# Kernel optimization log

Hardware: AMD Instinct MI355X
Metric: run time of the kernel (lower is better)

Reference implementation:

```python
import jax, jax.numpy as jnp
import numpy as np

MASK_THRESH = 0.9
USED_PENALTY = 1e8


def setup_inputs() -> dict:
    key = jax.random.key(0)
    k1, k2, k3, k4 = jax.random.split(key, 4)
    B, C, H, W = 16, 1, 128, 128
    P, L = 16, 6            # num_protos, num_objects
    T = P * L               # candidate templates per image
    x = jax.random.uniform(k1, (B, C, H, W), jnp.float32)
    templates = jax.random.uniform(k2, (B, T, C, H, W), jnp.float32)
    masks = jax.random.uniform(k3, (B, T, 1, H, W), jnp.float32)
    background = jax.random.uniform(k4, (C, H, W), jnp.float32)
    return {"x": x, "templates": templates, "masks": masks,
            "background": background, "num_objects": L}


def reference(x, templates, masks, background, num_objects):
    """Greedy template selection (use_empty=True) + scene composition.

    Faithful to DecompModel4._greedy_selection + compose_templates:
    at each of L steps, every candidate template is composed UNDER the
    already-selected objects (compose paints last index first), the MSE vs
    the image is computed, the argmin candidate is selected, and non-empty
    candidates are masked out for future steps. Final reconstruction paints
    selected objects over the background with object 0 on top.
    """
    B, T, C, H, W = templates.shape
    L = num_objects
    dt = templates.dtype

    # prepend the empty template (index 0), as in use_empty=True
    temps = jnp.concatenate([jnp.zeros((B, 1, C, H, W), dt), templates], axis=1)  # (B,T+1,C,H,W)
    msks = jnp.concatenate([jnp.zeros((B, 1, 1, H, W), dt), masks], axis=1)       # (B,T+1,1,H,W)
    Tp1 = T + 1
    bidx = jnp.arange(B)
    bg = background[None]                      # (1,C,H,W)

    # candidate-over-background image, constant across greedy steps
    cand_cov = msks > MASK_THRESH              # (B,T+1,1,H,W)
    cand_img = jnp.where(cand_cov, temps * msks, bg[:, None])  # (B,T+1,C,H,W)

    # running canvas of already-selected objects (earlier selections on top)
    used = jnp.zeros((B, Tp1), bool)
    top_val = jnp.zeros((B, C, H, W), dt)
    top_cov = jnp.zeros((B, 1, H, W), bool)

    for _ in range(L):
        # selected stack painted over each candidate-over-background
        cur = jnp.where(top_cov[:, None], top_val[:, None], cand_img)  # (B,T+1,C,H,W)
        err = jnp.mean((x[:, None] - cur) ** 2, axis=(2, 3, 4))        # (B,T+1)
        err = jnp.where(used, USED_PENALTY, err)
        cid = jnp.argmin(err, axis=1)                                  # (B,)
        # mark as used, except the empty template (id 0) stays reusable
        used = used | ((jnp.arange(Tp1)[None, :] == cid[:, None]) & (cid != 0)[:, None])
        sel_obj = temps[bidx, cid]     # (B,C,H,W)
        sel_msk = msks[bidx, cid]      # (B,1,H,W)
        new_cov = sel_msk > MASK_THRESH
        # new selection goes UNDER already-selected pixels
        top_val = jnp.where((~top_cov) & new_cov, sel_obj * sel_msk, top_val)
        top_cov = top_cov | new_cov

    reconstruction = jnp.where(top_cov, top_val, bg)   # (B,C,H,W)
    return reconstruction
```

## Files before the change

### kernel.cpp

```cpp
#include <hip/hip_runtime.h>

#define B    16
#define T    96
#define TP1  97
#define HW   16384
#define HW4  4096
#define LSEL 6
#define THRESH 0.9f
#define SEG  512
#define CAP  2048

#define WS_CONTRIB 0
#define WS_USED    8192
#define WS_COUNTS  16384
#define WS_COV     41984
#define WS_CIDX    304128
#define WS_CVAL    6595584
#define WS_NEEDED  (WS_CVAL + (size_t)B * T * CAP * 4)

__global__ __launch_bounds__(256) void compact_kernel(
    const float* __restrict__ x, const float* __restrict__ temps,
    const float* __restrict__ msks, const float* __restrict__ bg,
    unsigned short* __restrict__ cidx, float* __restrict__ cval,
    int* __restrict__ counts, float* __restrict__ contrib)
{
    int slot = blockIdx.x;
    int b = slot / T, t = slot - b * T;
    const float4* t4  = ((const float4*)temps) + (size_t)slot * HW4;
    const float4* m4  = ((const float4*)msks)  + (size_t)slot * HW4;
    const float4* x4  = ((const float4*)x)     + (size_t)b * HW4;
    const float4* bg4 = (const float4*)bg;
    int wv = threadIdx.x >> 6, lane = threadIdx.x & 63;
    unsigned long long below = lane ? (~0ULL >> (64 - lane)) : 0ULL;
    unsigned short* sidx = cidx + (size_t)slot * CAP + wv * SEG;
    float*          sval = cval + (size_t)slot * CAP + wv * SEG;

    int off = 0;
    float sum = 0.f;
    int ib = wv * 1024 + lane;

    #pragma unroll
    for (int it = 0; it < 16; it += 4) {
        float4 tv[4], mv[4], xv[4], bv[4];
        #pragma unroll
        for (int u = 0; u < 4; ++u) {
            int i = ib + (it + u) * 64;
            tv[u] = t4[i]; mv[u] = m4[i]; xv[u] = x4[i]; bv[u] = bg4[i];
        }
        #pragma unroll
        for (int u = 0; u < 4; ++u) {
            int pix = (ib + (it + u) * 64) * 4;
            bool p0 = mv[u].x > THRESH, p1 = mv[u].y > THRESH,
                 p2 = mv[u].z > THRESH, p3 = mv[u].w > THRESH;
            float a0 = xv[u].x - tv[u].x * mv[u].x, c0 = xv[u].x - bv[u].x;
            float a1 = xv[u].y - tv[u].y * mv[u].y, c1 = xv[u].y - bv[u].y;
            float a2 = xv[u].z - tv[u].z * mv[u].z, c2 = xv[u].z - bv[u].z;
            float a3 = xv[u].w - tv[u].w * mv[u].w, c3 = xv[u].w - bv[u].w;
            float v0 = a0*a0 - c0*c0, v1 = a1*a1 - c1*c1;
            float v2 = a2*a2 - c2*c2, v3 = a3*a3 - c3*c3;
            unsigned long long B0 = __ballot(p0), B1 = __ballot(p1);
            unsigned long long B2 = __ballot(p2), B3 = __ballot(p3);
            int n0 = __popcll(B0), n1 = __popcll(B1), n2 = __popcll(B2), n3 = __popcll(B3);
            if (p0) { int pos = off + __popcll(B0 & below);
                      if (pos < SEG) { sidx[pos] = (unsigned short)(pix+0); sval[pos] = v0; sum += v0; } }
            if (p1) { int pos = off + n0 + __popcll(B1 & below);
                      if (pos < SEG) { sidx[pos] = (unsigned short)(pix+1); sval[pos] = v1; sum += v1; } }
            if (p2) { int pos = off + n0 + n1 + __popcll(B2 & below);
                      if (pos < SEG) { sidx[pos] = (unsigned short)(pix+2); sval[pos] = v2; sum += v2; } }
            if (p3) { int pos = off + n0 + n1 + n2 + __popcll(B3 & below);
                      if (pos < SEG) { sidx[pos] = (unsigned short)(pix+3); sval[pos] = v3; sum += v3; } }
            off += n0 + n1 + n2 + n3;
        }
    }

    #pragma unroll
    for (int o = 32; o > 0; o >>= 1) sum += __shfl_down(sum, o, 64);
    __shared__ float s[4];
    if (lane == 0) s[wv] = sum;
    __syncthreads();
    if (threadIdx.x == 0) contrib[b * TP1 + t + 1] = s[0] + s[1] + s[2] + s[3];
    if (lane == 0) counts[slot * 4 + wv] = (off < SEG) ? off : SEG;
}

__global__ __launch_bounds__(256) void step_contrib_kernel(
    const unsigned short* __restrict__ cidx, const float* __restrict__ cval,
    const int* __restrict__ counts, const unsigned char* __restrict__ top_cov,
    float* __restrict__ contrib)
{
    int slot = blockIdx.x;
    int b = slot / T, t = slot - b * T;
    int wv = threadIdx.x >> 6, lane = threadIdx.x & 63;
    int n = counts[slot * 4 + wv];
    const unsigned short* sidx = cidx + (size_t)slot * CAP + wv * SEG;
    const float*          sval = cval + (size_t)slot * CAP + wv * SEG;
    const unsigned char*  cov  = top_cov + (size_t)b * HW;

    float sum = 0.f;
    for (int i = lane; i < n; i += 64) {
        unsigned short p = sidx[i];
        float v = sval[i];
        if (!cov[p]) sum += v;
    }
    #pragma unroll
    for (int o = 32; o > 0; o >>= 1) sum += __shfl_down(sum, o, 64);
    __shared__ float s[4];
    if (lane == 0) s[wv] = sum;
    __syncthreads();
    if (threadIdx.x == 0) contrib[b * TP1 + t + 1] = s[0] + s[1] + s[2] + s[3];
}

__global__ __launch_bounds__(256) void sel_upd_kernel(
    const float* __restrict__ contrib, const float* __restrict__ temps,
    const float* __restrict__ msks, const float* __restrict__ bg,
    unsigned long long* __restrict__ used, unsigned char* __restrict__ top_cov,
    float* __restrict__ out, int first, int last)
{
    int b = blockIdx.y, g = blockIdx.x;
    int tid = threadIdx.x;
    __shared__ float sv[128];
    __shared__ int   si[128];
    __shared__ int   sc;
    if (tid < 128) {
        float v = 3.0e38f;
        if (tid < TP1) {
            if (tid == 0) v = 0.0f;
            else {
                v = contrib[b * TP1 + tid];
                if (!first && ((used[b * 2 + (tid >> 6)] >> (tid & 63)) & 1ULL)) v = 1.0e8f;
            }
        }
        sv[tid] = v; si[tid] = tid;
    }
    __syncthreads();
    for (int o = 64; o > 0; o >>= 1) {
        if (tid < o) {
            float v2 = sv[tid + o]; int i2 = si[tid + o];
            if (v2 < sv[tid] || (v2 == sv[tid] && i2 < si[tid])) { sv[tid] = v2; si[tid] = i2; }
        }
        __syncthreads();
    }
    if (tid == 0) sc = si[0];
    __syncthreads();
    int c = sc;

    if (!last && g == 0 && tid == 0) {
        if (first) {
            used[b * 2 + 0] = (c != 0 && c < 64) ? (1ULL << c) : 0ULL;
            used[b * 2 + 1] = (c >= 64) ? (1ULL << (c - 64)) : 0ULL;
        } else if (c != 0) {
            atomicOr(&used[b * 2 + (c >> 6)], 1ULL << (c & 63));
        }
    }

    uchar4* covp = (uchar4*)(top_cov + (size_t)b * HW);
    float4* valp = (float4*)(out + (size_t)b * HW);
    const float4* bg4 = (const float4*)bg;
    int k0 = g * 1024;

    if (!last) {
        if (c != 0) {
            size_t tb = (size_t)(b * T + c - 1) * HW4;
            const float4* t4 = ((const float4*)temps) + tb;
            const float4* m4 = ((const float4*)msks) + tb;
            for (int k = k0 + tid; k < k0 + 1024; k += 256) {
                float4 mv = m4[k], tv = t4[k];
                uchar4 cv; float4 vv;
                if (first) {
                    cv.x = mv.x > THRESH; cv.y = mv.y > THRESH;
                    cv.z = mv.z > THRESH; cv.w = mv.w > THRESH;
                    vv.x = tv.x * mv.x; vv.y = tv.y * mv.y;
                    vv.z = tv.z * mv.z; vv.w = tv.w * mv.w;
                } else {
                    cv = covp[k]; vv = valp[k];
                    if (mv.x > THRESH && !cv.x) { vv.x = tv.x * mv.x; cv.x = 1; }
                    if (mv.y > THRESH && !cv.y) { vv.y = tv.y * mv.y; cv.y = 1; }
                    if (mv.z > THRESH && !cv.z) { vv.z = tv.z * mv.z; cv.z = 1; }
                    if (mv.w > THRESH && !cv.w) { vv.w = tv.w * mv.w; cv.w = 1; }
                }
                covp[k] = cv; valp[k] = vv;
            }
        } else if (first) {
            for (int k = k0 + tid; k < k0 + 1024; k += 256)
                covp[k] = make_uchar4(0, 0, 0, 0);
        }
    } else {
        if (c != 0) {
            size_t tb = (size_t)(b * T + c - 1) * HW4;
            const float4* t4 = ((const float4*)temps) + tb;
            const float4* m4 = ((const float4*)msks) + tb;
            for (int k = k0 + tid; k < k0 + 1024; k += 256) {
                float4 mv = m4[k], tv = t4[k];
                uchar4 cv = covp[k];
                float4 vv = valp[k];
                float4 bv = bg4[k];
                vv.x = cv.x ? vv.x : (mv.x > THRESH ? tv.x * mv.x : bv.x);
                vv.y = cv.y ? vv.y : (mv.y > THRESH ? tv.y * mv.y : bv.y);
                vv.z = cv.z ? vv.z : (mv.z > THRESH ? tv.z * mv.z : bv.z);
                vv.w = cv.w ? vv.w : (mv.w > THRESH ? tv.w * mv.w : bv.w);
                valp[k] = vv;
            }
        } else {
            for (int k = k0 + tid; k < k0 + 1024; k += 256) {
                uchar4 cv = covp[k];
                float4 vv = valp[k];
                float4 bv = bg4[k];
                if (!cv.x) vv.x = bv.x;
                if (!cv.y) vv.y = bv.y;
                if (!cv.z) vv.z = bv.z;
                if (!cv.w) vv.w = bv.w;
                valp[k] = vv;
            }
        }
    }
}

__global__ __launch_bounds__(256) void contrib_full_kernel(
    const float* __restrict__ x, const float* __restrict__ temps,
    const float* __restrict__ msks, const float* __restrict__ bg,
    const unsigned char* __restrict__ top_cov, float* __restrict__ contrib,
    int first)
{
    int b = blockIdx.x / T;
    int t = blockIdx.x % T;
    size_t base = (size_t)(b * T + t) * HW;
    const float4* t4  = (const float4*)(temps + base);
    const float4* m4  = (const float4*)(msks + base);
    const float4* x4  = (const float4*)(x + (size_t)b * HW);
    const float4* bg4 = (const float4*)bg;
    const uchar4* c4  = (const uchar4*)(top_cov + (size_t)b * HW);
    float sum = 0.f;
    #pragma unroll 4
    for (int i = threadIdx.x; i < HW4; i += 256) {
        float4 tv = t4[i], mv = m4[i], xv = x4[i], bv = bg4[i];
        uchar4 cv = first ? make_uchar4(0,0,0,0) : c4[i];
        if (mv.x > THRESH && !cv.x) { float d1 = xv.x - tv.x*mv.x, d2 = xv.x - bv.x; sum += d1*d1 - d2*d2; }
        if (mv.y > THRESH && !cv.y) { float d1 = xv.y - tv.y*mv.y, d2 = xv.y - bv.y; sum += d1*d1 - d2*d2; }
        if (mv.z > THRESH && !cv.z) { float d1 = xv.z - tv.z*mv.z, d2 = xv.z - bv.z; sum += d1*d1 - d2*d2; }
        if (mv.w > THRESH && !cv.w) { float d1 = xv.w - tv.w*mv.w, d2 = xv.w - bv.w; sum += d1*d1 - d2*d2; }
    }
    #pragma unroll
    for (int o = 32; o > 0; o >>= 1) sum += __shfl_down(sum, o, 64);
    __shared__ float s[4];
    int lane = threadIdx.x & 63, wid = threadIdx.x >> 6;
    if (lane == 0) s[wid] = sum;
    __syncthreads();
    if (threadIdx.x == 0)
        contrib[b * TP1 + t + 1] = s[0] + s[1] + s[2] + s[3];
}

extern "C" void kernel_launch(void* const* d_in, const int* in_sizes, int n_in,
                              void* d_out, int out_size, void* d_ws, size_t ws_size,
                              hipStream_t stream) {
    const float* x     = (const float*)d_in[0];
    const float* temps = (const float*)d_in[1];
    const float* msks  = (const float*)d_in[2];
    const float* bg    = (const float*)d_in[3];

    char* ws = (char*)d_ws;
    float*              contrib = (float*)(ws + WS_CONTRIB);
    unsigned long long* used    = (unsigned long long*)(ws + WS_USED);
    int*                counts  = (int*)(ws + WS_COUNTS);
    unsigned char*      top_cov = (unsigned char*)(ws + WS_COV);
    unsigned short*     cidx    = (unsigned short*)(ws + WS_CIDX);
    float*              cval    = (float*)(ws + WS_CVAL);
    float*              out     = (float*)d_out;

    if (ws_size >= WS_NEEDED) {
        compact_kernel<<<B * T, 256, 0, stream>>>(x, temps, msks, bg,
                                                  cidx, cval, counts, contrib);
        sel_upd_kernel<<<dim3(4, B), 256, 0, stream>>>(contrib, temps, msks, bg,
                                                       used, top_cov, out, 1, 0);
        for (int l = 1; l < LSEL - 1; ++l) {
            step_contrib_kernel<<<B * T, 256, 0, stream>>>(cidx, cval, counts, top_cov, contrib);
            sel_upd_kernel<<<dim3(4, B), 256, 0, stream>>>(contrib, temps, msks, bg,
                                                           used, top_cov, out, 0, 0);
        }
        step_contrib_kernel<<<B * T, 256, 0, stream>>>(cidx, cval, counts, top_cov, contrib);
        sel_upd_kernel<<<dim3(4, B), 256, 0, stream>>>(contrib, temps, msks, bg,
                                                       used, top_cov, out, 0, 1);
    } else {
        contrib_full_kernel<<<B * T, 256, 0, stream>>>(x, temps, msks, bg, top_cov, contrib, 1);
        sel_upd_kernel<<<dim3(4, B), 256, 0, stream>>>(contrib, temps, msks, bg,
                                                       used, top_cov, out, 1, 0);
        for (int l = 1; l < LSEL - 1; ++l) {
            contrib_full_kernel<<<B * T, 256, 0, stream>>>(x, temps, msks, bg, top_cov, contrib, 0);
            sel_upd_kernel<<<dim3(4, B), 256, 0, stream>>>(contrib, temps, msks, bg,
                                                           used, top_cov, out, 0, 0);
        }
        contrib_full_kernel<<<B * T, 256, 0, stream>>>(x, temps, msks, bg, top_cov, contrib, 0);
        sel_upd_kernel<<<dim3(4, B), 256, 0, stream>>>(contrib, temps, msks, bg,
                                                       used, top_cov, out, 0, 1);
    }
}
```

Baseline: 300.1 us.

## Fuse greedy selection into one persistent kernel with grid barriers

```diff
diff --git a/kernel.cpp b/kernel.cpp
--- a/kernel.cpp
+++ b/kernel.cpp
@@ -7,210 +7,232 @@
 #define HW4  4096
 #define LSEL 6
 #define THRESH 0.9f
-#define SEG  512
-#define CAP  2048
-
-#define WS_CONTRIB 0
-#define WS_USED    8192
-#define WS_COUNTS  16384
-#define WS_COV     41984
-#define WS_CIDX    304128
-#define WS_CVAL    6595584
-#define WS_NEEDED  (WS_CVAL + (size_t)B * T * CAP * 4)
-
-__global__ __launch_bounds__(256) void compact_kernel(
+#define SCAP  2048
+#define NBLK  256
+#define NSLOT (B * T)
+
+#define WS_BAR     0
+#define WS_SCOUNT  1024
+#define WS_CONTRIB 8192
+#define WS_USEDT   14848
+#define WS_COV     24576
+#define WS_CIDX    286720
+#define WS_CVAL    6578176
+#define WS_NEEDED  19161088ULL
+
+__global__ void init_kernel(unsigned long long* bar, unsigned* scount) {
+    int i = blockIdx.x * blockDim.x + threadIdx.x;
+    if (i < NSLOT) scount[i] = 0u;
+    if (i == 0) *bar = 0ULL;
+}
+
+__device__ __forceinline__ void grid_barrier(unsigned long long* bar,
+                                             unsigned long long target) {
+    __syncthreads();
+    __threadfence();
+    if (threadIdx.x == 0) {
+        __hip_atomic_fetch_add(bar, 1ULL, __ATOMIC_RELEASE, __HIP_MEMORY_SCOPE_AGENT);
+        while (__hip_atomic_load(bar, __ATOMIC_ACQUIRE, __HIP_MEMORY_SCOPE_AGENT) < target)
+            __builtin_amdgcn_s_sleep(2);
+    }
+    __syncthreads();
+    __threadfence();
+}
+
+__global__ __launch_bounds__(256, 1) void coop_kernel(
     const float* __restrict__ x, const float* __restrict__ temps,
     const float* __restrict__ msks, const float* __restrict__ bg,
     unsigned short* __restrict__ cidx, float* __restrict__ cval,
-    int* __restrict__ counts, float* __restrict__ contrib)
+    unsigned* __restrict__ scount, float* __restrict__ contrib,
+    unsigned char* __restrict__ cov, float* __restrict__ out,
+    unsigned long long* __restrict__ bar)
 {
-    int slot = blockIdx.x;
-    int b = slot / T, t = slot - b * T;
-    const float4* t4  = ((const float4*)temps) + (size_t)slot * HW4;
-    const float4* m4  = ((const float4*)msks)  + (size_t)slot * HW4;
-    const float4* x4  = ((const float4*)x)     + (size_t)b * HW4;
-    const float4* bg4 = (const float4*)bg;
-    int wv = threadIdx.x >> 6, lane = threadIdx.x & 63;
-    unsigned long long below = lane ? (~0ULL >> (64 - lane)) : 0ULL;
-    unsigned short* sidx = cidx + (size_t)slot * CAP + wv * SEG;
-    float*          sval = cval + (size_t)slot * CAP + wv * SEG;
-
-    int off = 0;
-    float sum = 0.f;
-    int ib = wv * 1024 + lane;
-
-    #pragma unroll
-    for (int it = 0; it < 16; it += 4) {
-        float4 tv[4], mv[4], xv[4], bv[4];
-        #pragma unroll
-        for (int u = 0; u < 4; ++u) {
-            int i = ib + (it + u) * 64;
-            tv[u] = t4[i]; mv[u] = m4[i]; xv[u] = x4[i]; bv[u] = bg4[i];
-        }
-        #pragma unroll
-        for (int u = 0; u < 4; ++u) {
-            int pix = (ib + (it + u) * 64) * 4;
-            bool p0 = mv[u].x > THRESH, p1 = mv[u].y > THRESH,
-                 p2 = mv[u].z > THRESH, p3 = mv[u].w > THRESH;
-            float a0 = xv[u].x - tv[u].x * mv[u].x, c0 = xv[u].x - bv[u].x;
-            float a1 = xv[u].y - tv[u].y * mv[u].y, c1 = xv[u].y - bv[u].y;
-            float a2 = xv[u].z - tv[u].z * mv[u].z, c2 = xv[u].z - bv[u].z;
-            float a3 = xv[u].w - tv[u].w * mv[u].w, c3 = xv[u].w - bv[u].w;
-            float v0 = a0*a0 - c0*c0, v1 = a1*a1 - c1*c1;
-            float v2 = a2*a2 - c2*c2, v3 = a3*a3 - c3*c3;
-            unsigned long long B0 = __ballot(p0), B1 = __ballot(p1);
-            unsigned long long B2 = __ballot(p2), B3 = __ballot(p3);
-            int n0 = __popcll(B0), n1 = __popcll(B1), n2 = __popcll(B2), n3 = __popcll(B3);
-            if (p0) { int pos = off + __popcll(B0 & below);
-                      if (pos < SEG) { sidx[pos] = (unsigned short)(pix+0); sval[pos] = v0; sum += v0; } }
-            if (p1) { int pos = off + n0 + __popcll(B1 & below);
-                      if (pos < SEG) { sidx[pos] = (unsigned short)(pix+1); sval[pos] = v1; sum += v1; } }
-            if (p2) { int pos = off + n0 + n1 + __popcll(B2 & below);
-                      if (pos < SEG) { sidx[pos] = (unsigned short)(pix+2); sval[pos] = v2; sum += v2; } }
-            if (p3) { int pos = off + n0 + n1 + n2 + __popcll(B3 & below);
-                      if (pos < SEG) { sidx[pos] = (unsigned short)(pix+3); sval[pos] = v3; sum += v3; } }
-            off += n0 + n1 + n2 + n3;
-        }
-    }
-
-    #pragma unroll
-    for (int o = 32; o > 0; o >>= 1) sum += __shfl_down(sum, o, 64);
-    __shared__ float s[4];
-    if (lane == 0) s[wv] = sum;
-    __syncthreads();
-    if (threadIdx.x == 0) contrib[b * TP1 + t + 1] = s[0] + s[1] + s[2] + s[3];
-    if (lane == 0) counts[slot * 4 + wv] = (off < SEG) ? off : SEG;
-}
-
-__global__ __launch_bounds__(256) void step_contrib_kernel(
-    const unsigned short* __restrict__ cidx, const float* __restrict__ cval,
-    const int* __restrict__ counts, const unsigned char* __restrict__ top_cov,
-    float* __restrict__ contrib)
-{
-    int slot = blockIdx.x;
-    int b = slot / T, t = slot - b * T;
-    int wv = threadIdx.x >> 6, lane = threadIdx.x & 63;
-    int n = counts[slot * 4 + wv];
-    const unsigned short* sidx = cidx + (size_t)slot * CAP + wv * SEG;
-    const float*          sval = cval + (size_t)slot * CAP + wv * SEG;
-    const unsigned char*  cov  = top_cov + (size_t)b * HW;
-
-    float sum = 0.f;
-    for (int i = lane; i < n; i += 64) {
-        unsigned short p = sidx[i];
-        float v = sval[i];
-        if (!cov[p]) sum += v;
-    }
-    #pragma unroll
-    for (int o = 32; o > 0; o >>= 1) sum += __shfl_down(sum, o, 64);
-    __shared__ float s[4];
-    if (lane == 0) s[wv] = sum;
-    __syncthreads();
-    if (threadIdx.x == 0) contrib[b * TP1 + t + 1] = s[0] + s[1] + s[2] + s[3];
-}
-
-__global__ __launch_bounds__(256) void sel_upd_kernel(
-    const float* __restrict__ contrib, const float* __restrict__ temps,
-    const float* __restrict__ msks, const float* __restrict__ bg,
-    unsigned long long* __restrict__ used, unsigned char* __restrict__ top_cov,
-    float* __restrict__ out, int first, int last)
-{
-    int b = blockIdx.y, g = blockIdx.x;
-    int tid = threadIdx.x;
+    const int bid = blockIdx.x;
+    const int tid = threadIdx.x;
+    const int lane = tid & 63, wv = tid >> 6;
+    const int b = bid >> 4;
+    const int chunk = bid & 15;
+
     __shared__ float sv[128];
     __shared__ int   si[128];
-    __shared__ int   sc;
-    if (tid < 128) {
-        float v = 3.0e38f;
-        if (tid < TP1) {
-            if (tid == 0) v = 0.0f;
-            else {
-                v = contrib[b * TP1 + tid];
-                if (!first && ((used[b * 2 + (tid >> 6)] >> (tid & 63)) & 1ULL)) v = 1.0e8f;
-            }
-        }
-        sv[tid] = v; si[tid] = tid;
-    }
-    __syncthreads();
-    for (int o = 64; o > 0; o >>= 1) {
-        if (tid < o) {
-            float v2 = sv[tid + o]; int i2 = si[tid + o];
-            if (v2 < sv[tid] || (v2 == sv[tid] && i2 < si[tid])) { sv[tid] = v2; si[tid] = i2; }
-        }
-        __syncthreads();
-    }
-    if (tid == 0) sc = si[0];
-    __syncthreads();
-    int c = sc;
-
-    if (!last && g == 0 && tid == 0) {
-        if (first) {
-            used[b * 2 + 0] = (c != 0 && c < 64) ? (1ULL << c) : 0ULL;
-            used[b * 2 + 1] = (c >= 64) ? (1ULL << (c - 64)) : 0ULL;
-        } else if (c != 0) {
-            atomicOr(&used[b * 2 + (c >> 6)], 1ULL << (c & 63));
-        }
-    }
-
-    uchar4* covp = (uchar4*)(top_cov + (size_t)b * HW);
-    float4* valp = (float4*)(out + (size_t)b * HW);
-    const float4* bg4 = (const float4*)bg;
-    int k0 = g * 1024;
-
-    if (!last) {
-        if (c != 0) {
-            size_t tb = (size_t)(b * T + c - 1) * HW4;
-            const float4* t4 = ((const float4*)temps) + tb;
-            const float4* m4 = ((const float4*)msks) + tb;
-            for (int k = k0 + tid; k < k0 + 1024; k += 256) {
-                float4 mv = m4[k], tv = t4[k];
-                uchar4 cv; float4 vv;
-                if (first) {
-                    cv.x = mv.x > THRESH; cv.y = mv.y > THRESH;
-                    cv.z = mv.z > THRESH; cv.w = mv.w > THRESH;
-                    vv.x = tv.x * mv.x; vv.y = tv.y * mv.y;
-                    vv.z = tv.z * mv.z; vv.w = tv.w * mv.w;
+    __shared__ int   scid;
+    __shared__ float sr[4];
+
+    bool my_used = false;
+    unsigned long long tgt = NBLK;
+
+    {
+        const float4* x4  = (const float4*)x + (size_t)b * HW4 + chunk * 256;
+        const float4* bgp = (const float4*)bg + chunk * 256;
+        float4 xv = x4[tid];
+        float4 bv = bgp[tid];
+        float4 d2;
+        d2.x = (xv.x - bv.x) * (xv.x - bv.x);
+        d2.y = (xv.y - bv.y) * (xv.y - bv.y);
+        d2.z = (xv.z - bv.z) * (xv.z - bv.z);
+        d2.w = (xv.w - bv.w) * (xv.w - bv.w);
+
+        const unsigned long long below = lane ? (~0ULL >> (64 - lane)) : 0ULL;
+        const float4* tbase = (const float4*)temps + (size_t)(b * T) * HW4 + chunk * 256 + tid;
+        const float4* mbase = (const float4*)msks  + (size_t)(b * T) * HW4 + chunk * 256 + tid;
+        const int gpix = (chunk * 256 + tid) * 4;
+
+        #pragma unroll 1
+        for (int t0 = 0; t0 < T; t0 += 8) {
+            float4 mv[8], tv[8];
+            #pragma unroll
+            for (int u = 0; u < 8; ++u) {
+                mv[u] = mbase[(size_t)(t0 + u) * HW4];
+                tv[u] = tbase[(size_t)(t0 + u) * HW4];
+            }
+            unsigned long long Ba0[8], Ba1[8], Ba2[8], Ba3[8];
+            int n0[8], n1[8], n2[8];
+            unsigned basew[8];
+            #pragma unroll
+            for (int u = 0; u < 8; ++u) {
+                Ba0[u] = __ballot(mv[u].x > THRESH);
+                Ba1[u] = __ballot(mv[u].y > THRESH);
+                Ba2[u] = __ballot(mv[u].z > THRESH);
+                Ba3[u] = __ballot(mv[u].w > THRESH);
+                n0[u] = __popcll(Ba0[u]); n1[u] = __popcll(Ba1[u]); n2[u] = __popcll(Ba2[u]);
+                int cnt4 = n0[u] + n1[u] + n2[u] + __popcll(Ba3[u]);
+                if (lane == 0)
+                    basew[u] = atomicAdd(&scount[b * T + t0 + u], (unsigned)cnt4);
+            }
+            #pragma unroll
+            for (int u = 0; u < 8; ++u) {
+                unsigned bw = (unsigned)__shfl((int)basew[u], 0, 64);
+                int slot = b * T + t0 + u;
+                unsigned short* ci = cidx + (size_t)slot * SCAP;
+                float*          cw = cval + (size_t)slot * SCAP;
+                float a0 = xv.x - tv[u].x * mv[u].x; float v0 = a0 * a0 - d2.x;
+                float a1 = xv.y - tv[u].y * mv[u].y; float v1 = a1 * a1 - d2.y;
+                float a2 = xv.z - tv[u].z * mv[u].z; float v2 = a2 * a2 - d2.z;
+                float a3 = xv.w - tv[u].w * mv[u].w; float v3 = a3 * a3 - d2.w;
+                if (mv[u].x > THRESH) {
+                    unsigned pos = bw + __popcll(Ba0[u] & below);
+                    if (pos < SCAP) { ci[pos] = (unsigned short)(gpix + 0); cw[pos] = v0; }
+                }
+                if (mv[u].y > THRESH) {
+                    unsigned pos = bw + n0[u] + __popcll(Ba1[u] & below);
+                    if (pos < SCAP) { ci[pos] = (unsigned short)(gpix + 1); cw[pos] = v1; }
+                }
+                if (mv[u].z > THRESH) {
+                    unsigned pos = bw + n0[u] + n1[u] + __popcll(Ba2[u] & below);
+                    if (pos < SCAP) { ci[pos] = (unsigned short)(gpix + 2); cw[pos] = v2; }
+                }
+                if (mv[u].w > THRESH) {
+                    unsigned pos = bw + n0[u] + n1[u] + n2[u] + __popcll(Ba3[u] & below);
+                    if (pos < SCAP) { ci[pos] = (unsigned short)(gpix + 3); cw[pos] = v3; }
+                }
+            }
+        }
+    }
+
+    grid_barrier(bar, tgt); tgt += NBLK;
+
+    for (int l = 1; l <= LSEL; ++l) {
+        {
+            const unsigned char* covb = cov + (size_t)b * HW;
+            #pragma unroll 1
+            for (int s = 0; s < 6; ++s) {
+                int t = chunk * 6 + s;
+                int slot = b * T + t;
+                unsigned n = scount[slot]; if (n > SCAP) n = SCAP;
+                const unsigned short* ci = cidx + (size_t)slot * SCAP;
+                const float*          cw = cval + (size_t)slot * SCAP;
+                float sum = 0.f;
+                if (l == 1) {
+                    for (unsigned i = tid; i < n; i += 256) sum += cw[i];
                 } else {
-                    cv = covp[k]; vv = valp[k];
-                    if (mv.x > THRESH && !cv.x) { vv.x = tv.x * mv.x; cv.x = 1; }
-                    if (mv.y > THRESH && !cv.y) { vv.y = tv.y * mv.y; cv.y = 1; }
-                    if (mv.z > THRESH && !cv.z) { vv.z = tv.z * mv.z; cv.z = 1; }
-                    if (mv.w > THRESH && !cv.w) { vv.w = tv.w * mv.w; cv.w = 1; }
-                }
-                covp[k] = cv; valp[k] = vv;
-            }
-        } else if (first) {
-            for (int k = k0 + tid; k < k0 + 1024; k += 256)
-                covp[k] = make_uchar4(0, 0, 0, 0);
-        }
-    } else {
-        if (c != 0) {
-            size_t tb = (size_t)(b * T + c - 1) * HW4;
-            const float4* t4 = ((const float4*)temps) + tb;
-            const float4* m4 = ((const float4*)msks) + tb;
-            for (int k = k0 + tid; k < k0 + 1024; k += 256) {
-                float4 mv = m4[k], tv = t4[k];
+                    for (unsigned i = tid; i < n; i += 256) {
+                        unsigned short p = ci[i];
+                        float v = cw[i];
+                        if (!covb[p]) sum += v;
+                    }
+                }
+                #pragma unroll
+                for (int o = 32; o > 0; o >>= 1) sum += __shfl_down(sum, o, 64);
+                __syncthreads();
+                if (lane == 0) sr[wv] = sum;
+                __syncthreads();
+                if (tid == 0) contrib[b * TP1 + t + 1] = sr[0] + sr[1] + sr[2] + sr[3];
+            }
+        }
+
+        grid_barrier(bar, tgt); tgt += NBLK;
+
+        {
+            const bool first = (l == 1), last = (l == LSEL);
+            if (tid < 128) {
+                float v = 3.0e38f;
+                if (tid < TP1)
+                    v = (tid == 0) ? 0.0f
+                                   : (my_used ? 1.0e8f : contrib[b * TP1 + tid]);
+                sv[tid] = v; si[tid] = tid;
+            }
+            __syncthreads();
+            for (int o = 64; o > 0; o >>= 1) {
+                if (tid < o) {
+                    float v2 = sv[tid + o]; int i2 = si[tid + o];
+                    if (v2 < sv[tid] || (v2 == sv[tid] && i2 < si[tid])) { sv[tid] = v2; si[tid] = i2; }
+                }
+                __syncthreads();
+            }
+            if (tid == 0) scid = si[0];
+            __syncthreads();
+            int c = scid;
+            if (tid == c && c != 0) my_used = true;
+
+            int k = chunk * 256 + tid;
+            uchar4* covp = (uchar4*)(cov + (size_t)b * HW);
+            float4* outp = (float4*)out + (size_t)b * HW4;
+
+            if (!last) {
+                if (c != 0) {
+                    size_t tb = (size_t)(b * T + c - 1) * HW4 + k;
+                    float4 mv = ((const float4*)msks)[tb];
+                    float4 tv = ((const float4*)temps)[tb];
+                    uchar4 cv; float4 vv;
+                    if (first) {
+                        cv.x = mv.x > THRESH; cv.y = mv.y > THRESH;
+                        cv.z = mv.z > THRESH; cv.w = mv.w > THRESH;
+                        vv.x = tv.x * mv.x; vv.y = tv.y * mv.y;
+                        vv.z = tv.z * mv.z; vv.w = tv.w * mv.w;
+                    } else {
+                        cv = covp[k]; vv = outp[k];
+                        if (mv.x > THRESH && !cv.x) { vv.x = tv.x * mv.x; cv.x = 1; }
+                        if (mv.y > THRESH && !cv.y) { vv.y = tv.y * mv.y; cv.y = 1; }
+                        if (mv.z > THRESH && !cv.z) { vv.z = tv.z * mv.z; cv.z = 1; }
+                        if (mv.w > THRESH && !cv.w) { vv.w = tv.w * mv.w; cv.w = 1; }
+                    }
+                    covp[k] = cv; outp[k] = vv;
+                } else if (first) {
+                    covp[k] = make_uchar4(0, 0, 0, 0);
+                }
+            } else {
+                float4 bv = ((const float4*)bg)[k];
                 uchar4 cv = covp[k];
-                float4 vv = valp[k];
-                float4 bv = bg4[k];
-                vv.x = cv.x ? vv.x : (mv.x > THRESH ? tv.x * mv.x : bv.x);
-                vv.y = cv.y ? vv.y : (mv.y > THRESH ? tv.y * mv.y : bv.y);
-                vv.z = cv.z ? vv.z : (mv.z > THRESH ? tv.z * mv.z : bv.z);
-                vv.w = cv.w ? vv.w : (mv.w > THRESH ? tv.w * mv.w : bv.w);
-                valp[k] = vv;
-            }
-        } else {
-            for (int k = k0 + tid; k < k0 + 1024; k += 256) {
-                uchar4 cv = covp[k];
-                float4 vv = valp[k];
-                float4 bv = bg4[k];
-                if (!cv.x) vv.x = bv.x;
-                if (!cv.y) vv.y = bv.y;
-                if (!cv.z) vv.z = bv.z;
-                if (!cv.w) vv.w = bv.w;
-                valp[k] = vv;
-            }
-        }
+                float4 vv = outp[k];
+                if (c != 0) {
+                    size_t tb = (size_t)(b * T + c - 1) * HW4 + k;
+                    float4 mv = ((const float4*)msks)[tb];
+                    float4 tv = ((const float4*)temps)[tb];
+                    vv.x = cv.x ? vv.x : (mv.x > THRESH ? tv.x * mv.x : bv.x);
+                    vv.y = cv.y ? vv.y : (mv.y > THRESH ? tv.y * mv.y : bv.y);
+                    vv.z = cv.z ? vv.z : (mv.z > THRESH ? tv.z * mv.z : bv.z);
+                    vv.w = cv.w ? vv.w : (mv.w > THRESH ? tv.w * mv.w : bv.w);
+                } else {
+                    if (!cv.x) vv.x = bv.x;
+                    if (!cv.y) vv.y = bv.y;
+                    if (!cv.z) vv.z = bv.z;
+                    if (!cv.w) vv.w = bv.w;
+                }
+                outp[k] = vv;
+            }
+        }
+
+        if (l < LSEL) { grid_barrier(bar, tgt); tgt += NBLK; }
     }
 }
 
@@ -248,6 +270,111 @@
         contrib[b * TP1 + t + 1] = s[0] + s[1] + s[2] + s[3];
 }
 
+__global__ __launch_bounds__(256) void sel_upd_kernel(
+    const float* __restrict__ contrib, const float* __restrict__ temps,
+    const float* __restrict__ msks, const float* __restrict__ bg,
+    int* __restrict__ usedt, unsigned char* __restrict__ top_cov,
+    float* __restrict__ out, int l)
+{
+    const bool first = (l == 1), last = (l == LSEL);
+    int b = blockIdx.y, g = blockIdx.x;
+    int tid = threadIdx.x;
+    __shared__ float sv[128];
+    __shared__ int   si[128];
+    __shared__ int   sc;
+    if (tid < 128) {
+        float v = 3.0e38f;
+        if (tid < TP1) {
+            if (tid == 0) v = 0.0f;
+            else {
+                v = contrib[b * TP1 + tid];
+                if (!first) {
+                    int u = usedt[b * TP1 + tid];
+                    if (u != 0 && u < l) v = 1.0e8f;
+                }
+            }
+        }
+        sv[tid] = v; si[tid] = tid;
+    }
+    __syncthreads();
+    for (int o = 64; o > 0; o >>= 1) {
+        if (tid < o) {
+            float v2 = sv[tid + o]; int i2 = si[tid + o];
+            if (v2 < sv[tid] || (v2 == sv[tid] && i2 < si[tid])) { sv[tid] = v2; si[tid] = i2; }
+        }
+        __syncthreads();
+    }
+    if (tid == 0) sc = si[0];
+    __syncthreads();
+    int c = sc;
+
+    if (!last && g == 0) {
+        if (first) { if (tid < TP1) usedt[b * TP1 + tid] = (tid == c && c != 0) ? 1 : 0; }
+        else if (c != 0 && tid == 0) usedt[b * TP1 + c] = l;
+    }
+
+    uchar4* covp = (uchar4*)(top_cov + (size_t)b * HW);
+    float4* valp = (float4*)(out + (size_t)b * HW);
+    const float4* bg4 = (const float4*)bg;
+    int k0 = g * 1024;
+
+    if (!last) {
+        if (c != 0) {
+            size_t tb = (size_t)(b * T + c - 1) * HW4;
+            const float4* t4 = ((const float4*)temps) + tb;
+            const float4* m4 = ((const float4*)msks) + tb;
+            for (int k = k0 + tid; k < k0 + 1024; k += 256) {
+                float4 mv = m4[k], tv = t4[k];
+                uchar4 cv; float4 vv;
+                if (first) {
+                    cv.x = mv.x > THRESH; cv.y = mv.y > THRESH;
+                    cv.z = mv.z > THRESH; cv.w = mv.w > THRESH;
+                    vv.x = tv.x * mv.x; vv.y = tv.y * mv.y;
+                    vv.z = tv.z * mv.z; vv.w = tv.w * mv.w;
+                } else {
+                    cv = covp[k]; vv = valp[k];
+                    if (mv.x > THRESH && !cv.x) { vv.x = tv.x * mv.x; cv.x = 1; }
+                    if (mv.y > THRESH && !cv.y) { vv.y = tv.y * mv.y; cv.y = 1; }
+                    if (mv.z > THRESH && !cv.z) { vv.z = tv.z * mv.z; cv.z = 1; }
+                    if (mv.w > THRESH && !cv.w) { vv.w = tv.w * mv.w; cv.w = 1; }
+                }
+                covp[k] = cv; valp[k] = vv;
+            }
+        } else if (first) {
+            for (int k = k0 + tid; k < k0 + 1024; k += 256)
+                covp[k] = make_uchar4(0, 0, 0, 0);
+        }
+    } else {
+        if (c != 0) {
+            size_t tb = (size_t)(b * T + c - 1) * HW4;
+            const float4* t4 = ((const float4*)temps) + tb;
+            const float4* m4 = ((const float4*)msks) + tb;
+            for (int k = k0 + tid; k < k0 + 1024; k += 256) {
+                float4 mv = m4[k], tv = t4[k];
+                uchar4 cv = covp[k];
+                float4 vv = valp[k];
+                float4 bv = bg4[k];
+                vv.x = cv.x ? vv.x : (mv.x > THRESH ? tv.x * mv.x : bv.x);
+                vv.y = cv.y ? vv.y : (mv.y > THRESH ? tv.y * mv.y : bv.y);
+                vv.z = cv.z ? vv.z : (mv.z > THRESH ? tv.z * mv.z : bv.z);
+                vv.w = cv.w ? vv.w : (mv.w > THRESH ? tv.w * mv.w : bv.w);
+                valp[k] = vv;
+            }
+        } else {
+            for (int k = k0 + tid; k < k0 + 1024; k += 256) {
+                uchar4 cv = covp[k];
+                float4 vv = valp[k];
+                float4 bv = bg4[k];
+                if (!cv.x) vv.x = bv.x;
+                if (!cv.y) vv.y = bv.y;
+                if (!cv.z) vv.z = bv.z;
+                if (!cv.w) vv.w = bv.w;
+                valp[k] = vv;
+            }
+        }
+    }
+}
+
 extern "C" void kernel_launch(void* const* d_in, const int* in_sizes, int n_in,
                               void* d_out, int out_size, void* d_ws, size_t ws_size,
                               hipStream_t stream) {
@@ -257,38 +384,25 @@
     const float* bg    = (const float*)d_in[3];
 
     char* ws = (char*)d_ws;
+    unsigned long long* bar     = (unsigned long long*)(ws + WS_BAR);
+    unsigned*           scount  = (unsigned*)(ws + WS_SCOUNT);
     float*              contrib = (float*)(ws + WS_CONTRIB);
-    unsigned long long* used    = (unsigned long long*)(ws + WS_USED);
-    int*                counts  = (int*)(ws + WS_COUNTS);
-    unsigned char*      top_cov = (unsigned char*)(ws + WS_COV);
+    int*                usedt   = (int*)(ws + WS_USEDT);
+    unsigned char*      cov     = (unsigned char*)(ws + WS_COV);
     unsigned short*     cidx    = (unsigned short*)(ws + WS_CIDX);
     float*              cval    = (float*)(ws + WS_CVAL);
     float*              out     = (float*)d_out;
 
     if (ws_size >= WS_NEEDED) {
-        compact_kernel<<<B * T, 256, 0, stream>>>(x, temps, msks, bg,
-                                                  cidx, cval, counts, contrib);
-        sel_upd_kernel<<<dim3(4, B), 256, 0, stream>>>(contrib, temps, msks, bg,
-                                                       used, top_cov, out, 1, 0);
-        for (int l = 1; l < LSEL - 1; ++l) {
-            step_contrib_kernel<<<B * T, 256, 0, stream>>>(cidx, cval, counts, top_cov, contrib);
+        init_kernel<<<6, 256, 0, stream>>>(bar, scount);
+        coop_kernel<<<NBLK, 256, 0, stream>>>(x, temps, msks, bg, cidx, cval,
+                                              scount, contrib, cov, out, bar);
+    } else {
+        for (int l = 1; l <= LSEL; ++l) {
+            contrib_full_kernel<<<B * T, 256, 0, stream>>>(x, temps, msks, bg, cov,
+                                                           contrib, l == 1 ? 1 : 0);
             sel_upd_kernel<<<dim3(4, B), 256, 0, stream>>>(contrib, temps, msks, bg,
-                                                           used, top_cov, out, 0, 0);
-        }
-        step_contrib_kernel<<<B * T, 256, 0, stream>>>(cidx, cval, counts, top_cov, contrib);
-        sel_upd_kernel<<<dim3(4, B), 256, 0, stream>>>(contrib, temps, msks, bg,
-                                                       used, top_cov, out, 0, 1);
-    } else {
-        contrib_full_kernel<<<B * T, 256, 0, stream>>>(x, temps, msks, bg, top_cov, contrib, 1);
-        sel_upd_kernel<<<dim3(4, B), 256, 0, stream>>>(contrib, temps, msks, bg,
-                                                       used, top_cov, out, 1, 0);
-        for (int l = 1; l < LSEL - 1; ++l) {
-            contrib_full_kernel<<<B * T, 256, 0, stream>>>(x, temps, msks, bg, top_cov, contrib, 0);
-            sel_upd_kernel<<<dim3(4, B), 256, 0, stream>>>(contrib, temps, msks, bg,
-                                                           used, top_cov, out, 0, 0);
-        }
-        contrib_full_kernel<<<B * T, 256, 0, stream>>>(x, temps, msks, bg, top_cov, contrib, 0);
-        sel_upd_kernel<<<dim3(4, B), 256, 0, stream>>>(contrib, temps, msks, bg,
-                                                       used, top_cov, out, 0, 1);
-    }
-}
+                                                           usedt, cov, out, l);
+        }
+    }
+}
```

Result: slower. 1.048 ms (+249.3%).
